# Kernel tuning notes

Measured on AMD Instinct MI355X. Metric: run time of the kernel, lower is better.

## Reference

```python
import jax, jax.numpy as jnp
import numpy as np
import math

# Spherical conv per Esteves et al. spherical CNNs (sph_conv_batch):
#   1) spherical-harmonic transform of input on an n x n equiangular grid
#   2) per-degree multiply by zonal filter coeffs w[c_in, l, c_out],
#      scaled by 2*pi*sqrt(4*pi/(2l+1))
#   3) inverse transform, plus bias add.
# Implemented as FFT over longitude + Legendre quadrature over colatitude.

BATCH, N_GRID, C_IN, C_OUT = 64, 32, 128, 128
L_MAX = N_GRID // 2  # spherical-harmonic bandwidth


def _legendre_Q(L, n):
    """Normalized associated Legendre N_lm * P_l^m(cos theta_j).
    Returns Q (L, 2L-1, n) with m index offset by L-1, and theta (n,)."""
    theta = np.pi * (np.arange(n) + 0.5) / n
    x, sx = np.cos(theta), np.sin(theta)
    P = np.zeros((L, L, n))
    P[0, 0] = 1.0
    for m in range(1, L):
        P[m, m] = -(2 * m - 1) * sx * P[m - 1, m - 1]
    for m in range(L - 1):
        P[m + 1, m] = (2 * m + 1) * x * P[m, m]
        for l in range(m + 2, L):
            P[l, m] = ((2 * l - 1) * x * P[l - 1, m] - (l + m - 1) * P[l - 2, m]) / (l - m)
    Q = np.zeros((L, 2 * L - 1, n))
    for l in range(L):
        for m in range(l + 1):
            Nlm = np.sqrt((2 * l + 1) / (4 * np.pi)
                          * np.exp(math.lgamma(l - m + 1) - math.lgamma(l + m + 1)))
            Q[l, L - 1 + m] = Nlm * P[l, m]
            Q[l, L - 1 - m] = ((-1) ** m) * Nlm * P[l, m]
    return Q, theta


def _sph_conv(inputs, weights, bias):
    b, n, _, c_in = inputs.shape
    L = weights.shape[1]
    Q, theta = _legendre_Q(L, n)
    # quadrature: sin(theta)*dtheta*dphi, dtheta = pi/n, dphi = 2*pi/n
    wj = np.sin(theta) * (np.pi / n) * (2.0 * np.pi / n)
    Qw = jnp.asarray(Q * wj, dtype=jnp.float32).astype(jnp.complex64)   # (L, 2L-1, n)
    Qs = jnp.asarray(Q, dtype=jnp.float32).astype(jnp.complex64)
    ms = np.arange(-(L - 1), L) % n  # 2L-1 distinct FFT bins
    # forward SHT: FFT over phi then Legendre quadrature over theta
    F = jnp.fft.fft(inputs.astype(jnp.complex64), axis=2)[:, :, ms, :]  # (b, n, 2L-1, c_in)
    coef = jnp.einsum('lmj,bjmc->blmc', Qw, F)                          # (b, L, 2L-1, c_in)
    # zonal spectral filter: per-degree scale 2*pi*sqrt(4*pi/(2l+1))
    scale = jnp.asarray(2.0 * np.pi * np.sqrt(4.0 * np.pi / (2.0 * np.arange(L) + 1.0)),
                        jnp.float32)
    chat = jnp.einsum('blmi,ilo->blmo', coef, weights.astype(jnp.complex64))
    chat = chat * scale[None, :, None, None]
    # inverse SHT: Legendre synthesis then inverse FFT over phi
    G = jnp.einsum('blmo,lmj->bjmo', chat, Qs)                          # (b, n, 2L-1, c_out)
    Gfull = jnp.zeros((b, n, n, G.shape[-1]), jnp.complex64).at[:, :, ms, :].set(G)
    out = jnp.real(jnp.fft.ifft(Gfull, axis=2)) * n                    # (b, n, n, c_out)
    return out + bias


def setup_inputs() -> dict:
    key = jax.random.key(0)
    k1, k2 = jax.random.split(key)
    std = 2.0 / (2.0 * np.pi * np.sqrt(L_MAX * C_IN))
    inputs = jax.random.normal(k1, (BATCH, N_GRID, N_GRID, C_IN), jnp.float32)
    weights = jax.random.normal(k2, (C_IN, L_MAX, C_OUT), jnp.float32) * std
    bias = jnp.zeros((1, 1, 1, C_OUT), jnp.float32)
    return {"inputs": inputs, "weights": weights, "bias": bias}


def reference(inputs, weights, bias):
    return _sph_conv(inputs, weights, bias)
```

## Files before the change

kernel.cpp:

```cpp
#include <hip/hip_runtime.h>
#include <hip/hip_bf16.h>
#include <math.h>


#define NPAIR 136

typedef __attribute__((ext_vector_type(8))) short short8;
typedef __attribute__((ext_vector_type(4))) float f32x4;
#define MFMA16(A, B, C) __builtin_amdgcn_mfma_f32_16x16x32_bf16(A, B, C, 0, 0, 0)

static __device__ __forceinline__ float us2f(unsigned int u) {
  union { unsigned int i; float f; } v; v.i = u << 16; return v.f;
}
static __device__ __forceinline__ unsigned short f2us(float f) {
  __hip_bfloat16 h = __float2bfloat16(f);
  return *(unsigned short*)&h;
}
static __device__ __forceinline__ float lo_f(unsigned int pk) {
  union { unsigned int i; float f; } v; v.i = pk << 16; return v.f;
}
static __device__ __forceinline__ float hi_f(unsigned int pk) {
  union { unsigned int i; float f; } v; v.i = pk & 0xffff0000u; return v.f;
}
static __device__ __forceinline__ unsigned int packbf(float a, float b) {
  return (unsigned int)f2us(a) | ((unsigned int)f2us(b) << 16);
}

__device__ __align__(16) unsigned short g_atab_h[NPAIR * 32];
__device__ __align__(16) float          g_stab[NPAIR * 32];

static __device__ __forceinline__ int detect_fp32(const void* xin) {
  const unsigned short* u = (const unsigned short*)xin;
  int lane = threadIdx.x & 63;
  int big = 0;
#pragma unroll
  for (int q = 0; q < 4; ++q) {
    float v = us2f((unsigned int)u[lane * 8 + q * 2]);
    if (!(fabsf(v) <= 1e3f)) big = 1;
  }
  unsigned long long mask = __ballot(big);
  return (__popcll(mask) >= 16) ? 1 : 0;
}

static __device__ __forceinline__ size_t chat_q_byte(int b, int oq, int u, int esz) {
  int wpr = 8 * esz;
  int s = u / wpr, w = u % wpr;
  return ((size_t)b * 131072 + (size_t)s * 128 + oq * 32) * (size_t)esz + (size_t)w * 4;
}
static __device__ __forceinline__ size_t coef_byte(int b, int h, int u, int esz) {
  int wpr = 16 * esz;
  int s = 544 / esz + u / wpr, w = u % wpr;
  return ((size_t)b * 131072 + (size_t)s * 128 + h * 64) * (size_t)esz + (size_t)w * 4;
}

#define DEF_TRIG \
  constexpr float CT[32] = { \
    1.0f, 0.98078528f, 0.92387953f, 0.83146961f, 0.70710678f, 0.55557023f, \
    0.38268343f, 0.19509032f, 0.0f, -0.19509032f, -0.38268343f, -0.55557023f, \
    -0.70710678f, -0.83146961f, -0.92387953f, -0.98078528f, -1.0f, \
    -0.98078528f, -0.92387953f, -0.83146961f, -0.70710678f, -0.55557023f, \
    -0.38268343f, -0.19509032f, 0.0f, 0.19509032f, 0.38268343f, 0.55557023f, \
    0.70710678f, 0.83146961f, 0.92387953f, 0.98078528f }; \
  constexpr float ST[32] = { \
    0.0f, 0.19509032f, 0.38268343f, 0.55557023f, 0.70710678f, 0.83146961f, \
    0.92387953f, 0.98078528f, 1.0f, 0.98078528f, 0.92387953f, 0.83146961f, \
    0.70710678f, 0.55557023f, 0.38268343f, 0.19509032f, 0.0f, \
    -0.19509032f, -0.38268343f, -0.55557023f, -0.70710678f, -0.83146961f, \
    -0.92387953f, -0.98078528f, -1.0f, -0.98078528f, -0.92387953f, \
    -0.83146961f, -0.70710678f, -0.55557023f, -0.38268343f, -0.19509032f }

__global__ void k_init() {
  const int pair = blockIdx.x, j = threadIdx.x;
  int m = 0;
#pragma unroll
  for (int mm = 1; mm < 16; ++mm) {
    int off = mm * 16 - (mm * (mm - 1)) / 2;
    if (off <= pair) m = mm;
  }
  const int l = m + (pair - (m * 16 - (m * (m - 1)) / 2));
  double theta = M_PI * (j + 0.5) / 32.0;
  double x = cos(theta), sx = sin(theta);
  double wj = sx * (M_PI / 32.0) * (2.0 * M_PI / 32.0);
  double pmm = 1.0;
  for (int k = 1; k <= m; ++k) pmm *= -(2.0 * k - 1.0) * sx;
  double p = pmm, pl1 = 0.0, pl2 = 0.0;
  for (int ll = m; ll <= l; ++ll) {
    if (ll == m)          p = pmm;
    else if (ll == m + 1) p = (2.0 * m + 1.0) * x * pmm;
    else                  p = ((2.0 * ll - 1.0) * x * pl1 - (double)(ll + m - 1) * pl2) / (double)(ll - m);
    pl2 = pl1; pl1 = p;
  }
  double r = 1.0;
  for (int k = l - m + 1; k <= l + m; ++k) r *= (double)k;
  double Nlm = sqrt((2.0 * l + 1.0) / (4.0 * M_PI) / r);
  g_atab_h[pair * 32 + j] = f2us((float)(Nlm * p * wj));
  g_stab[pair * 32 + j] = (float)(Nlm * p * (2.0 * M_PI * sqrt(4.0 * M_PI / (2.0 * l + 1.0)))
                                  * (m ? 2.0 : 1.0));
}

__global__ __launch_bounds__(256) void k_fwd(const void* __restrict__ xin,
                                             char* __restrict__ outbuf) {
  const int fp32m = detect_fp32(xin);
  const int esz = fp32m ? 4 : 2;
  __shared__ __align__(16) unsigned short xs[32 * 264];
  __shared__ __align__(16) unsigned int   fsp[128 * 36];
  const int blk = blockIdx.x;
  const int b = (blk & 7) | (((blk >> 7) & 7) << 3);
  const int cq = (blk >> 3) & 15;
  const int t = threadIdx.x;
  if (fp32m) {
    const float* xf = (const float*)xin;
#pragma unroll
    for (int it = 0; it < 8; ++it) {
      int i = t + it * 256;
      int s = i >> 1, hf = i & 1;
      float4 v = *(const float4*)(xf + ((size_t)b * 1024 + s) * 128 + cq * 8 + hf * 4);
      int p = s & 31, j = s >> 5;
      *(uint2*)&xs[p * 264 + j * 8 + hf * 4] = make_uint2(packbf(v.x, v.y), packbf(v.z, v.w));
    }
  } else {
    const unsigned short* xh = (const unsigned short*)xin;
#pragma unroll
    for (int it = 0; it < 4; ++it) {
      int s = t + it * 256;
      uint4 v = *(const uint4*)(xh + ((size_t)b * 1024 + s) * 128 + cq * 8);
      int p = s & 31, j = s >> 5;
      *(uint4*)&xs[p * 264 + j * 8] = v;
    }
  }
  __syncthreads();
  {
    DEF_TRIG;
    const int j = t >> 3, c = t & 7, rb = j * 8 + c;
    float x0  = us2f((unsigned int)xs[rb]);
    float x16 = us2f((unsigned int)xs[16 * 264 + rb]);
    float sp[16], dm[16];
#pragma unroll
    for (int p = 1; p <= 15; ++p) {
      float a  = us2f((unsigned int)xs[p * 264 + rb]);
      float bq = us2f((unsigned int)xs[(32 - p) * 264 + rb]);
      sp[p] = a + bq; dm[p] = a - bq;
    }
#pragma unroll
    for (int mi = 0; mi < 16; ++mi) {
      float re = x0 + ((mi & 1) ? -x16 : x16);
      float im = 0.f;
#pragma unroll
      for (int p = 1; p <= 15; ++p) {
        re += sp[p] * CT[(mi * p) & 31];
        im -= dm[p] * ST[(mi * p) & 31];
      }
      fsp[(mi * 8 + c) * 36 + j] = packbf(re, im);
    }
  }
  __syncthreads();
  {
    const int m = t >> 4, c = (t >> 1) & 7, jh = t & 1;
    const int cg = cq * 8 + c, h = cg >> 6, cl = cg & 63;
    const int base = m * 16 - (m * (m - 1)) / 2;
    uint4 F[4];
#pragma unroll
    for (int q = 0; q < 4; ++q)
      F[q] = *(const uint4*)&fsp[(m * 8 + c) * 36 + jh * 16 + q * 4];
    for (int l = m; l < 16; ++l) {
      int pair = base + (l - m);
      float sr = 0.f, si = 0.f;
#pragma unroll
      for (int q = 0; q < 2; ++q) {
        uint4 a = *(const uint4*)&g_atab_h[pair * 32 + jh * 16 + q * 8];
        float a0 = us2f(a.x & 0xffff), a1 = us2f(a.x >> 16);
        float a2 = us2f(a.y & 0xffff), a3 = us2f(a.y >> 16);
        float a4 = us2f(a.z & 0xffff), a5 = us2f(a.z >> 16);
        float a6 = us2f(a.w & 0xffff), a7 = us2f(a.w >> 16);
        uint4 f0 = F[2 * q], f1 = F[2 * q + 1];
        sr += a0 * lo_f(f0.x) + a1 * lo_f(f0.y) + a2 * lo_f(f0.z) + a3 * lo_f(f0.w)
            + a4 * lo_f(f1.x) + a5 * lo_f(f1.y) + a6 * lo_f(f1.z) + a7 * lo_f(f1.w);
        si += a0 * hi_f(f0.x) + a1 * hi_f(f0.y) + a2 * hi_f(f0.z) + a3 * hi_f(f0.w)
            + a4 * hi_f(f1.x) + a5 * hi_f(f1.y) + a6 * hi_f(f1.z) + a7 * hi_f(f1.w);
      }
      sr += __shfl_xor(sr, 1, 64);
      si += __shfl_xor(si, 1, 64);
      if (jh == 0) {
        int u = pair * 64 + cl;
        *(unsigned int*)(outbuf + coef_byte(b, h, u, esz)) = packbf(sr, si);
      }
    }
  }
}

__global__ __launch_bounds__(256) void k_chan(char* __restrict__ outbuf,
                                              const void* __restrict__ Wv,
                                              const void* __restrict__ xin) {
  const int fp32m = detect_fp32(xin);
  const int esz = fp32m ? 4 : 2;
  const int pair = blockIdx.x >> 2;
  const int bh = (blockIdx.x >> 1) & 1, otile = blockIdx.x & 1;
  int m = 0;
#pragma unroll
  for (int mm = 1; mm < 16; ++mm) {
    int off = mm * 16 - (mm * (mm - 1)) / 2;
    if (off <= pair) m = mm;
  }
  const int l = m + (pair - (m * 16 - (m * (m - 1)) / 2));
  __shared__ __align__(16) unsigned short Xr[32 * 136];
  __shared__ __align__(16) unsigned short Xi[32 * 136];
  __shared__ __align__(16) unsigned short Wt[64 * 136];
  const int t = threadIdx.x;
  for (int i = t; i < 4096; i += 256) {
    int bl = i >> 7, c = i & 127;
    unsigned int pk = *(const unsigned int*)(outbuf +
        coef_byte(bh * 32 + bl, c >> 6, pair * 64 + (c & 63), esz));
    Xr[bl * 136 + c] = (unsigned short)(pk & 0xffff);
    Xi[bl * 136 + c] = (unsigned short)(pk >> 16);
  }
  for (int i = t; i < 1024; i += 256) {
    int c = i >> 3, og = i & 7;
    size_t widx = (size_t)c * 2048 + l * 128 + otile * 64 + og * 8;
    if (fp32m) {
      const float* Wf = (const float*)Wv;
      float4 f0 = *(const float4*)(Wf + widx);
      float4 f1 = *(const float4*)(Wf + widx + 4);
      Wt[(og * 8 + 0) * 136 + c] = f2us(f0.x); Wt[(og * 8 + 1) * 136 + c] = f2us(f0.y);
      Wt[(og * 8 + 2) * 136 + c] = f2us(f0.z); Wt[(og * 8 + 3) * 136 + c] = f2us(f0.w);
      Wt[(og * 8 + 4) * 136 + c] = f2us(f1.x); Wt[(og * 8 + 5) * 136 + c] = f2us(f1.y);
      Wt[(og * 8 + 6) * 136 + c] = f2us(f1.z); Wt[(og * 8 + 7) * 136 + c] = f2us(f1.w);
    } else {
      const unsigned short* Wh = (const unsigned short*)Wv;
      uint4 v = *(const uint4*)(Wh + widx);
      Wt[(og * 8 + 0) * 136 + c] = (unsigned short)(v.x & 0xffff);
      Wt[(og * 8 + 1) * 136 + c] = (unsigned short)(v.x >> 16);
      Wt[(og * 8 + 2) * 136 + c] = (unsigned short)(v.y & 0xffff);
      Wt[(og * 8 + 3) * 136 + c] = (unsigned short)(v.y >> 16);
      Wt[(og * 8 + 4) * 136 + c] = (unsigned short)(v.z & 0xffff);
      Wt[(og * 8 + 5) * 136 + c] = (unsigned short)(v.z >> 16);
      Wt[(og * 8 + 6) * 136 + c] = (unsigned short)(v.w & 0xffff);
      Wt[(og * 8 + 7) * 136 + c] = (unsigned short)(v.w >> 16);
    }
  }
  __syncthreads();
  const int wv = t >> 6, lane = t & 63;
  const int col = lane & 15, quad = lane >> 4;
  const int mtile = wv & 1, ng = wv >> 1;
  f32x4 accR0 = {0.f, 0.f, 0.f, 0.f}, accI0 = accR0, accR1 = accR0, accI1 = accR0;
#pragma unroll
  for (int kc = 0; kc < 4; ++kc) {
    short8 Ar = *(const short8*)&Xr[(mtile * 16 + col) * 136 + kc * 32 + quad * 8];
    short8 Ai = *(const short8*)&Xi[(mtile * 16 + col) * 136 + kc * 32 + quad * 8];
    short8 B0 = *(const short8*)&Wt[(ng * 32 + col) * 136 + kc * 32 + quad * 8];
    short8 B1 = *(const short8*)&Wt[(ng * 32 + 16 + col) * 136 + kc * 32 + quad * 8];
    accR0 = MFMA16(Ar, B0, accR0);
    accI0 = MFMA16(Ai, B0, accI0);
    accR1 = MFMA16(Ar, B1, accR1);
    accI1 = MFMA16(Ai, B1, accI1);
  }
#pragma unroll
  for (int reg = 0; reg < 4; ++reg) {
    int bb = bh * 32 + mtile * 16 + quad * 4 + reg;
    int o0 = otile * 64 + ng * 32 + col;
    int o1 = o0 + 16;
    *(unsigned int*)(outbuf + chat_q_byte(bb, o0 >> 5, pair * 32 + (o0 & 31), esz)) =
        packbf(accR0[reg], accI0[reg]);
    *(unsigned int*)(outbuf + chat_q_byte(bb, o1 >> 5, pair * 32 + (o1 & 31), esz)) =
        packbf(accR1[reg], accI1[reg]);
  }
}

__global__ __launch_bounds__(512) void k_bwd(char* __restrict__ outbuf,
                                             const void* __restrict__ biasv,
                                             const void* __restrict__ xin) {
  const int fp32m = detect_fp32(xin);
  const int esz = fp32m ? 4 : 2;
  __shared__ __align__(16) unsigned int chs[NPAIR * 32];
  __shared__ float stb[NPAIR * 32];
  const int b = blockIdx.x >> 2, oq = blockIdx.x & 3;
  const int t = threadIdx.x;
  for (int i = t; i < NPAIR * 8; i += 512)
    ((uint4*)chs)[i] = *(const uint4*)(outbuf + chat_q_byte(b, oq, i * 4, esz));
  for (int i = t; i < NPAIR * 32; i += 512) stb[i] = g_stab[i];
  const int j = t >> 4, ou = t & 15;
  __syncthreads();

  DEF_TRIG;
#pragma unroll 1
  for (int un = 0; un < 2; ++un) {
    const int ol = ou + un * 16;
    const int o = oq * 32 + ol;
    float bv = fp32m ? ((const float*)biasv)[o]
                     : us2f((unsigned int)((const unsigned short*)biasv)[o]);
    float Gr[16], Gi[16];
#pragma unroll
    for (int mm = 0; mm < 16; ++mm) { Gr[mm] = 0.f; Gi[mm] = 0.f; }
    int pair = 0;
#pragma unroll
    for (int mm = 0; mm < 16; ++mm) {
#pragma unroll
      for (int l = mm; l < 16; ++l) {
        float s = stb[pair * 32 + j];
        unsigned int cv = chs[pair * 32 + ol];
        Gr[mm] += s * lo_f(cv);
        Gi[mm] += s * hi_f(cv);
        ++pair;
      }
    }
#pragma unroll
    for (int pp = 0; pp <= 16; ++pp) {
      float A = 0.f, Bv = 0.f;
#pragma unroll
      for (int mm = 0; mm < 16; ++mm) {
        A  += Gr[mm] * CT[(mm * pp) & 31];
        Bv += Gi[mm] * ST[(mm * pp) & 31];
      }
      int p2 = (32 - pp) & 31;
      size_t e1 = (size_t)b * 131072 + (size_t)(j * 32 + pp) * 128 + o;
      size_t e2 = (size_t)b * 131072 + (size_t)(j * 32 + p2) * 128 + o;
      if (fp32m) {
        *(float*)(outbuf + e1 * 4) = bv + A - Bv;
        *(float*)(outbuf + e2 * 4) = bv + A + Bv;
      } else {
        *(unsigned short*)(outbuf + e1 * 2) = f2us(bv + A - Bv);
        *(unsigned short*)(outbuf + e2 * 2) = f2us(bv + A + Bv);
      }
    }
  }
}

extern "C" void kernel_launch(void* const* d_in, const int* in_sizes, int n_in,
                              void* d_out, int out_size, void* d_ws, size_t ws_size,
                              hipStream_t stream) {
  const void* xin  = d_in[0];
  const void* W    = d_in[1];
  const void* bias = d_in[2];
  char* out = (char*)d_out;

  hipLaunchKernelGGL(k_init, dim3(NPAIR), dim3(32),  0, stream);
  hipLaunchKernelGGL(k_fwd,  dim3(1024),  dim3(256), 0, stream, xin, out);
  hipLaunchKernelGGL(k_chan, dim3(544),   dim3(256), 0, stream, out, W, xin);
  hipLaunchKernelGGL(k_bwd,  dim3(256),   dim3(512), 0, stream, out, bias, xin);
}
```

Baseline: 132.9 us.

## Transpose backward-pass tables to pair-contiguous layout and use 1024-thread blocks

The Legendre synthesis tables and per-block spectral coefficients in the backward kernel are transposed so pairs are contiguous per latitude/channel, padded to 140. This allows float4/uint4 LDS reads instead of scalar strided ones. The block grows to 1024 threads, so each thread handles one output channel instead of looping over two, which removes the serial loop. Risks include register pressure at 1024 threads and bank conflicts from the transposed scatter stores into shared memory.

```diff
diff --git a/kernel.cpp b/kernel.cpp
--- a/kernel.cpp
+++ b/kernel.cpp
@@ -4,6 +4,7 @@
 
 
 #define NPAIR 136
+#define PADC 140
 
 typedef __attribute__((ext_vector_type(8))) short short8;
 typedef __attribute__((ext_vector_type(4))) float f32x4;
@@ -27,7 +28,7 @@
 }
 
 __device__ __align__(16) unsigned short g_atab_h[NPAIR * 32];
-__device__ __align__(16) float          g_stab[NPAIR * 32];
+__device__ __align__(16) float          g_stab[32 * PADC];
 
 static __device__ __forceinline__ int detect_fp32(const void* xin) {
   const unsigned short* u = (const unsigned short*)xin;
@@ -94,8 +95,8 @@
   for (int k = l - m + 1; k <= l + m; ++k) r *= (double)k;
   double Nlm = sqrt((2.0 * l + 1.0) / (4.0 * M_PI) / r);
   g_atab_h[pair * 32 + j] = f2us((float)(Nlm * p * wj));
-  g_stab[pair * 32 + j] = (float)(Nlm * p * (2.0 * M_PI * sqrt(4.0 * M_PI / (2.0 * l + 1.0)))
-                                  * (m ? 2.0 : 1.0));
+  g_stab[j * PADC + pair] = (float)(Nlm * p * (2.0 * M_PI * sqrt(4.0 * M_PI / (2.0 * l + 1.0)))
+                                    * (m ? 2.0 : 1.0));
 }
 
 __global__ __launch_bounds__(256) void k_fwd(const void* __restrict__ xin,
@@ -265,61 +266,73 @@
   }
 }
 
-__global__ __launch_bounds__(512) void k_bwd(char* __restrict__ outbuf,
-                                             const void* __restrict__ biasv,
-                                             const void* __restrict__ xin) {
+__global__ __launch_bounds__(1024) void k_bwd(char* __restrict__ outbuf,
+                                              const void* __restrict__ biasv,
+                                              const void* __restrict__ xin) {
   const int fp32m = detect_fp32(xin);
   const int esz = fp32m ? 4 : 2;
-  __shared__ __align__(16) unsigned int chs[NPAIR * 32];
-  __shared__ float stb[NPAIR * 32];
+  __shared__ __align__(16) unsigned int chs[32 * PADC];
+  __shared__ __align__(16) float        stb[32 * PADC];
   const int b = blockIdx.x >> 2, oq = blockIdx.x & 3;
   const int t = threadIdx.x;
-  for (int i = t; i < NPAIR * 8; i += 512)
-    ((uint4*)chs)[i] = *(const uint4*)(outbuf + chat_q_byte(b, oq, i * 4, esz));
-  for (int i = t; i < NPAIR * 32; i += 512) stb[i] = g_stab[i];
-  const int j = t >> 4, ou = t & 15;
+  for (int i = t; i < NPAIR * 8; i += 1024) {
+    uint4 v = *(const uint4*)(outbuf + chat_q_byte(b, oq, i * 4, esz));
+    const int pair = i >> 3, ol0 = (i & 7) * 4;
+    chs[(ol0 + 0) * PADC + pair] = v.x;
+    chs[(ol0 + 1) * PADC + pair] = v.y;
+    chs[(ol0 + 2) * PADC + pair] = v.z;
+    chs[(ol0 + 3) * PADC + pair] = v.w;
+  }
+  for (int i = t; i < 32 * PADC / 4; i += 1024)
+    ((float4*)stb)[i] = ((const float4*)g_stab)[i];
+  const int j = t >> 5, ol = t & 31;
+  const int o = oq * 32 + ol;
+  const float bv = fp32m ? ((const float*)biasv)[o]
+                         : us2f((unsigned int)((const unsigned short*)biasv)[o]);
   __syncthreads();
 
-  DEF_TRIG;
-#pragma unroll 1
-  for (int un = 0; un < 2; ++un) {
-    const int ol = ou + un * 16;
-    const int o = oq * 32 + ol;
-    float bv = fp32m ? ((const float*)biasv)[o]
-                     : us2f((unsigned int)((const unsigned short*)biasv)[o]);
-    float Gr[16], Gi[16];
-#pragma unroll
-    for (int mm = 0; mm < 16; ++mm) { Gr[mm] = 0.f; Gi[mm] = 0.f; }
+  float Gr[16], Gi[16];
+#pragma unroll
+  for (int mm = 0; mm < 16; ++mm) { Gr[mm] = 0.f; Gi[mm] = 0.f; }
+  {
+    float4 s4 = {0.f, 0.f, 0.f, 0.f};
+    uint4  c4 = {0u, 0u, 0u, 0u};
     int pair = 0;
 #pragma unroll
     for (int mm = 0; mm < 16; ++mm) {
 #pragma unroll
       for (int l = mm; l < 16; ++l) {
-        float s = stb[pair * 32 + j];
-        unsigned int cv = chs[pair * 32 + ol];
+        if ((pair & 3) == 0) {
+          s4 = *(const float4*)&stb[j * PADC + pair];
+          c4 = *(const uint4*)&chs[ol * PADC + pair];
+        }
+        const int r = pair & 3;
+        const float        s  = (r == 0) ? s4.x : (r == 1) ? s4.y : (r == 2) ? s4.z : s4.w;
+        const unsigned int cv = (r == 0) ? c4.x : (r == 1) ? c4.y : (r == 2) ? c4.z : c4.w;
         Gr[mm] += s * lo_f(cv);
         Gi[mm] += s * hi_f(cv);
         ++pair;
       }
     }
-#pragma unroll
-    for (int pp = 0; pp <= 16; ++pp) {
-      float A = 0.f, Bv = 0.f;
-#pragma unroll
-      for (int mm = 0; mm < 16; ++mm) {
-        A  += Gr[mm] * CT[(mm * pp) & 31];
-        Bv += Gi[mm] * ST[(mm * pp) & 31];
-      }
-      int p2 = (32 - pp) & 31;
-      size_t e1 = (size_t)b * 131072 + (size_t)(j * 32 + pp) * 128 + o;
-      size_t e2 = (size_t)b * 131072 + (size_t)(j * 32 + p2) * 128 + o;
-      if (fp32m) {
-        *(float*)(outbuf + e1 * 4) = bv + A - Bv;
-        *(float*)(outbuf + e2 * 4) = bv + A + Bv;
-      } else {
-        *(unsigned short*)(outbuf + e1 * 2) = f2us(bv + A - Bv);
-        *(unsigned short*)(outbuf + e2 * 2) = f2us(bv + A + Bv);
-      }
+  }
+  DEF_TRIG;
+#pragma unroll
+  for (int pp = 0; pp <= 16; ++pp) {
+    float A = 0.f, Bv = 0.f;
+#pragma unroll
+    for (int mm = 0; mm < 16; ++mm) {
+      A  += Gr[mm] * CT[(mm * pp) & 31];
+      Bv += Gi[mm] * ST[(mm * pp) & 31];
+    }
+    const int p2 = (32 - pp) & 31;
+    size_t e1 = (size_t)b * 131072 + (size_t)(j * 32 + pp) * 128 + o;
+    size_t e2 = (size_t)b * 131072 + (size_t)(j * 32 + p2) * 128 + o;
+    if (fp32m) {
+      *(float*)(outbuf + e1 * 4) = bv + A - Bv;
+      *(float*)(outbuf + e2 * 4) = bv + A + Bv;
+    } else {
+      *(unsigned short*)(outbuf + e1 * 2) = f2us(bv + A - Bv);
+      *(unsigned short*)(outbuf + e2 * 2) = f2us(bv + A + Bv);
     }
   }
 }
@@ -332,8 +345,8 @@
   const void* bias = d_in[2];
   char* out = (char*)d_out;
 
-  hipLaunchKernelGGL(k_init, dim3(NPAIR), dim3(32),  0, stream);
-  hipLaunchKernelGGL(k_fwd,  dim3(1024),  dim3(256), 0, stream, xin, out);
-  hipLaunchKernelGGL(k_chan, dim3(544),   dim3(256), 0, stream, out, W, xin);
-  hipLaunchKernelGGL(k_bwd,  dim3(256),   dim3(512), 0, stream, out, bias, xin);
-}
+  hipLaunchKernelGGL(k_init, dim3(NPAIR), dim3(32),   0, stream);
+  hipLaunchKernelGGL(k_fwd,  dim3(1024),  dim3(256),  0, stream, xin, out);
+  hipLaunchKernelGGL(k_chan, dim3(544),   dim3(256),  0, stream, out, W, xin);
+  hipLaunchKernelGGL(k_bwd,  dim3(256),   dim3(1024), 0, stream, out, bias, xin);
+}
```

Result: faster. 122.1 us (-8.1%).
